# Kernel tuning notes

Measured on AMD Instinct MI355X. Metric: run time of the kernel, lower is better.

The kernel has to match this reference:

```python
import jax, jax.numpy as jnp
import numpy as np

STRIDES = (8.0, 16.0, 32.0)


def _decode_level(feat, W, b, stride, level):
    # feat: [bs, C, ny, nx]; W: [85, C]; b: [85]
    bs, _, ny, nx = feat.shape
    # 1x1 conv == channel contraction; output laid out as [bs, ny, nx, 85]
    p = jnp.einsum('bchw,oc->bhwo', feat, W) + b
    y = jax.nn.sigmoid(p)
    xv = jnp.arange(nx, dtype=y.dtype)            # broadcasts over last spatial dim
    yv = jnp.arange(ny, dtype=y.dtype)[:, None]   # broadcasts over row dim
    power = jnp.asarray(2.0 ** level, dtype=y.dtype)
    d = (y[..., :4] * 2.0) ** 2 * power           # dx1, dy1, dx2, dy2
    x1 = (xv + 1.0 - d[..., 0]) * stride
    y1 = (yv + 1.0 - d[..., 1]) * stride
    x2 = (xv + d[..., 2]) * stride
    y2 = (yv + d[..., 3]) * stride
    # xyxy -> xywh
    box = jnp.stack([(x1 + x2) * 0.5, (y1 + y2) * 0.5, x2 - x1, y2 - y1], axis=-1)
    out = jnp.concatenate([box, y[..., 4:]], axis=-1)  # [bs, ny, nx, 85]
    return out.reshape(bs, ny * nx, out.shape[-1])


def setup_inputs() -> dict:
    key = jax.random.key(0)
    ks = jax.random.split(key, 9)
    f32 = jnp.float32
    return {
        'x0': jax.random.normal(ks[0], (16, 256, 80, 80), dtype=f32),
        'x1': jax.random.normal(ks[1], (16, 512, 40, 40), dtype=f32),
        'x2': jax.random.normal(ks[2], (16, 1024, 20, 20), dtype=f32),
        'W0': jax.random.normal(ks[3], (85, 256), dtype=f32) * 0.05,
        'b0': jax.random.normal(ks[4], (85,), dtype=f32) * 0.05,
        'W1': jax.random.normal(ks[5], (85, 512), dtype=f32) * 0.05,
        'b1': jax.random.normal(ks[6], (85,), dtype=f32) * 0.05,
        'W2': jax.random.normal(ks[7], (85, 1024), dtype=f32) * 0.05,
        'b2': jax.random.normal(ks[8], (85,), dtype=f32) * 0.05,
    }


def reference(x0, x1, x2, W0, b0, W1, b1, W2, b2):
    feats = (x0, x1, x2)
    Ws = (W0, W1, W2)
    bs_ = (b0, b1, b2)
    z = [_decode_level(feats[i], Ws[i], bs_[i], STRIDES[i], i) for i in range(3)]
    return jnp.concatenate(z, axis=1)  # [bs, 8400, 85]
```

## Files before the change

kernel.cpp:

```cpp
#include <hip/hip_runtime.h>
#include <cstdint>


typedef __attribute__((ext_vector_type(8))) short bf16x8;
typedef __attribute__((ext_vector_type(4))) float f32x4;

constexpr int KS0 = 8, KS1 = 16, KS2 = 32;
constexpr int F0 = 6 * KS0, F1 = 6 * KS1, F2 = 6 * KS2;
constexpr int FOFF0 = 0, FOFF1 = F0, FOFF2 = F0 + F1;
constexpr int NFRAG = F0 + F1 + F2;
constexpr size_t BIAS_OFF = 0;
constexpr size_t BPK_OFF  = 1152;
constexpr size_t WS_NEED  = BPK_OFF + (size_t)NFRAG * 64 * 16;

__device__ __forceinline__ unsigned short f2bf(float f) {
    union { float f; unsigned u; } v; v.f = f;
    unsigned r = v.u + 0x7FFF + ((v.u >> 16) & 1);
    return (unsigned short)(r >> 16);
}

__global__ __launch_bounds__(256) void prep_pack(
    const float* __restrict__ W0, const float* __restrict__ W1,
    const float* __restrict__ W2,
    const float* __restrict__ b0, const float* __restrict__ b1,
    const float* __restrict__ b2,
    unsigned char* __restrict__ ws)
{
    int t = blockIdx.x * 256 + threadIdx.x;
    if (t < 288) {
        int lvl = t / 96, o = t % 96;
        const float* bp = (lvl == 0) ? b0 : (lvl == 1) ? b1 : b2;
        ((float*)(ws + BIAS_OFF))[t] = (o < 85) ? bp[o] : 0.0f;
    }
    if (t >= NFRAG * 64) return;
    int frag = t >> 6, l = t & 63;
    int C; const float* W; int f;
    if (frag < FOFF1)      { C = 256;  W = W0; f = frag;         }
    else if (frag < FOFF2) { C = 512;  W = W1; f = frag - FOFF1; }
    else                   { C = 1024; W = W2; f = frag - FOFF2; }
    int ks = f / 6, n = f % 6;
    int o  = n * 16 + (l & 15);
    int c0 = ks * 32 + (l >> 4) * 8;
    bf16x8 r;
#pragma unroll
    for (int e = 0; e < 8; ++e)
        r[e] = (o < 85) ? (short)f2bf(W[(size_t)o * C + c0 + e]) : (short)0;
    ((bf16x8*)(ws + BPK_OFF))[frag * 64 + l] = r;
}

template <int C, int HW, int NX, int LEVEL, int AOFF, int KSTEPS, int FOFF>
__device__ __forceinline__ void mfma_level(
    const float* __restrict__ feat, const unsigned char* __restrict__ ws,
    float* __restrict__ out, int blk, uint4* __restrict__ Bsm )
{
    const int tid = threadIdx.x;
    const int w   = tid >> 6;
    const int l   = tid & 63;
    const int col = l & 15;
    const int kg  = l >> 4;

    const int p0s[2] = { blk * 128 + w * 32, blk * 128 + w * 32 + 16 };
    const float* fb[2];
    int bidx[2], hw0[2];
#pragma unroll
    for (int s = 0; s < 2; ++s) {
        int b   = p0s[s] / HW;
        bidx[s] = b;
        hw0[s]  = p0s[s] - b * HW;
        fb[s]   = feat + (size_t)b * C * HW + hw0[s];
    }

    const float* bias = (const float*)(ws + BIAS_OFF) + LEVEL * 96;
    const uint4* bsrc = (const uint4*)(ws + BPK_OFF) + (size_t)FOFF * 64;

    f32x4 acc[2][6];
#pragma unroll
    for (int n = 0; n < 6; ++n) {
        float bv = bias[n * 16 + col];
        f32x4 z = { bv, bv, bv, bv };
        acc[0][n] = z;
        acc[1][n] = z;
    }

    {
        const uint4* s = bsrc;
        Bsm[tid] = s[tid];
        if (tid < 128) Bsm[256 + tid] = s[256 + tid];
    }
    __syncthreads();

    int cur = 0;
    for (int ks = 0; ks < KSTEPS; ++ks) {
        float fl0[8], fl1[8];
        const float* p0p = fb[0] + col + (size_t)(ks * 32 + kg * 8) * HW;
        const float* p1p = fb[1] + col + (size_t)(ks * 32 + kg * 8) * HW;
#pragma unroll
        for (int e = 0; e < 8; ++e) fl0[e] = p0p[(size_t)e * HW];
#pragma unroll
        for (int e = 0; e < 8; ++e) fl1[e] = p1p[(size_t)e * HW];

        uint4 s0, s1;
        const int ksn = (ks + 1 < KSTEPS) ? ks + 1 : ks;
        {
            const uint4* s = bsrc + (size_t)ksn * 384;
            s0 = s[tid];
            if (tid < 128) s1 = s[256 + tid];
        }

        bf16x8 a0, a1;
#pragma unroll
        for (int e = 0; e < 8; ++e) a0[e] = (short)f2bf(fl0[e]);
#pragma unroll
        for (int e = 0; e < 8; ++e) a1[e] = (short)f2bf(fl1[e]);

        const bf16x8* bl = (const bf16x8*)(Bsm + (size_t)cur * 384);
#pragma unroll
        for (int n = 0; n < 6; ++n) {
            bf16x8 bq = bl[n * 64 + l];
            acc[0][n] = __builtin_amdgcn_mfma_f32_16x16x32_bf16(a0, bq, acc[0][n], 0, 0, 0);
            acc[1][n] = __builtin_amdgcn_mfma_f32_16x16x32_bf16(a1, bq, acc[1][n], 0, 0, 0);
        }

        if (ks + 1 < KSTEPS) {
            uint4* d = Bsm + (size_t)(cur ^ 1) * 384;
            d[tid] = s0;
            if (tid < 128) d[256 + tid] = s1;
        }
        __syncthreads();
        cur ^= 1;
    }

    constexpr float S  = (float)(8 << LEVEL);
    constexpr float P4 = 4.0f * (float)(1 << LEVEL);
#pragma unroll
    for (int s = 0; s < 2; ++s) {
        const int b = bidx[s];
#pragma unroll
        for (int j = 0; j < 4; ++j) {
            const int hw = hw0[s] + kg * 4 + j;
            float sg[6];
#pragma unroll
            for (int n = 0; n < 6; ++n) {
                float v = acc[s][n][j];
                sg[n] = __builtin_amdgcn_rcpf(1.0f + __expf(-v));
            }
            const int grp = l & 48;
            float y0 = __shfl(sg[0], grp + 0);
            float y1 = __shfl(sg[0], grp + 1);
            float y2 = __shfl(sg[0], grp + 2);
            float y3 = __shfl(sg[0], grp + 3);
            float wx = (float)(hw % NX);
            float wy = (float)(hw / NX);
            float d0 = y0 * y0 * P4, d1 = y1 * y1 * P4;
            float d2 = y2 * y2 * P4, d3 = y3 * y3 * P4;
            float x1 = (wx + 1.0f - d0) * S;
            float yA = (wy + 1.0f - d1) * S;
            float x2 = (wx + d2) * S;
            float yB = (wy + d3) * S;
            float bx = (x1 + x2) * 0.5f, by = (yA + yB) * 0.5f;
            float bw = x2 - x1,          bh = yB - yA;
            sg[0] = (col == 0) ? bx : (col == 1) ? by
                  : (col == 2) ? bw : (col == 3) ? bh : sg[0];
            float* op = out + ((size_t)b * 8400 + AOFF + hw) * 85;
#pragma unroll
            for (int n = 0; n < 6; ++n) {
                int o = n * 16 + col;
                if (o < 85) op[o] = sg[n];
            }
        }
    }
}

__global__ __launch_bounds__(256, 4) void detect_mfma(
    const float* __restrict__ x0, const float* __restrict__ x1,
    const float* __restrict__ x2,
    const unsigned char* __restrict__ ws, float* __restrict__ out)
{
    __shared__ uint4 Bsm[2 * 384];
    int blk = blockIdx.x;
    if (blk < 50)       mfma_level<1024, 400,  20, 2, 8000, KS2, FOFF2>(x2, ws, out, blk,       Bsm);
    else if (blk < 250) mfma_level<512,  1600, 40, 1, 6400, KS1, FOFF1>(x1, ws, out, blk - 50,  Bsm);
    else                mfma_level<256,  6400, 80, 0, 0,    KS0, FOFF0>(x0, ws, out, blk - 250, Bsm);
}

template <int C, int HW, int NX, int LEVEL, int ONUM, bool BOX>
__device__ __forceinline__ void decode_path_fb(
    const float* __restrict__ feat, const float* __restrict__ Wm,
    const float* __restrict__ bias, float* __restrict__ out,
    int o_lo_in, int pos)
{
    const int o_lo = __builtin_amdgcn_readfirstlane(o_lo_in);
    const int b  = pos / HW;
    const int hw = pos - b * HW;
    const float* fp = feat + (size_t)b * (C * HW) + hw;
    float acc[ONUM];
#pragma unroll
    for (int j = 0; j < ONUM; ++j) acc[j] = bias[o_lo + j];
#pragma unroll 4
    for (int c = 0; c < C; ++c) {
        float fv = fp[(size_t)c * HW];
#pragma unroll
        for (int j = 0; j < ONUM; ++j)
            acc[j] = fmaf(fv, Wm[(o_lo + j) * C + c], acc[j]);
    }
#pragma unroll
    for (int j = 0; j < ONUM; ++j)
        acc[j] = __builtin_amdgcn_rcpf(1.0f + __expf(-acc[j]));
    constexpr float S = (float)(8 << LEVEL);
    constexpr int AOFF = (LEVEL == 0) ? 0 : ((LEVEL == 1) ? 6400 : 8000);
    float* op = out + ((size_t)b * 8400 + AOFF + hw) * 85 + o_lo;
    if constexpr (BOX) {
        constexpr float P4 = 4.0f * (float)(1 << LEVEL);
        float wx = (float)(hw % NX), wy = (float)(hw / NX);
        float d0 = acc[0] * acc[0] * P4, d1 = acc[1] * acc[1] * P4;
        float d2 = acc[2] * acc[2] * P4, d3 = acc[3] * acc[3] * P4;
        float x1 = (wx + 1.0f - d0) * S, y1 = (wy + 1.0f - d1) * S;
        float x2 = (wx + d2) * S,        y2 = (wy + d3) * S;
        op[0] = (x1 + x2) * 0.5f; op[1] = (y1 + y2) * 0.5f;
        op[2] = x2 - x1;          op[3] = y2 - y1;
#pragma unroll
        for (int j = 4; j < ONUM; ++j) op[j] = acc[j];
    } else {
#pragma unroll
        for (int j = 0; j < ONUM; ++j) op[j] = acc[j];
    }
}

template <int C, int HW, int NX, int LEVEL>
__device__ __forceinline__ void level_block_fb(
    const float* __restrict__ feat, const float* __restrict__ Wm,
    const float* __restrict__ bias, float* __restrict__ out, int bb)
{
    const int wave = threadIdx.x >> 6, lane = threadIdx.x & 63;
    const int pos = bb * 64 + lane;
    if      (wave == 0) decode_path_fb<C, HW, NX, LEVEL, 22, true >(feat, Wm, bias, out, 0,  pos);
    else if (wave == 1) decode_path_fb<C, HW, NX, LEVEL, 22, false>(feat, Wm, bias, out, 22, pos);
    else if (wave == 2) decode_path_fb<C, HW, NX, LEVEL, 22, false>(feat, Wm, bias, out, 44, pos);
    else                decode_path_fb<C, HW, NX, LEVEL, 19, false>(feat, Wm, bias, out, 66, pos);
}

__global__ __launch_bounds__(256) void detect_fallback(
    const float* __restrict__ x0, const float* __restrict__ x1,
    const float* __restrict__ x2,
    const float* __restrict__ w0, const float* __restrict__ w1,
    const float* __restrict__ w2,
    const float* __restrict__ b0, const float* __restrict__ b1,
    const float* __restrict__ b2, float* __restrict__ out)
{
    const int blk = blockIdx.x;
    if (blk < 100)      level_block_fb<1024, 400,  20, 2>(x2, w2, b2, out, blk);
    else if (blk < 500) level_block_fb<512,  1600, 40, 1>(x1, w1, b1, out, blk - 100);
    else                level_block_fb<256,  6400, 80, 0>(x0, w0, b0, out, blk - 500);
}

extern "C" void kernel_launch(void* const* d_in, const int* in_sizes, int n_in,
                              void* d_out, int out_size, void* d_ws, size_t ws_size,
                              hipStream_t stream)
{
    const float* x0 = (const float*)d_in[0];
    const float* x1 = (const float*)d_in[1];
    const float* x2 = (const float*)d_in[2];
    const float* W0 = (const float*)d_in[3];
    const float* b0 = (const float*)d_in[4];
    const float* W1 = (const float*)d_in[5];
    const float* b1 = (const float*)d_in[6];
    const float* W2 = (const float*)d_in[7];
    const float* b2 = (const float*)d_in[8];
    float* out = (float*)d_out;

    if (ws_size >= WS_NEED) {
        unsigned char* ws = (unsigned char*)d_ws;
        prep_pack<<<(NFRAG * 64 + 255) / 256, 256, 0, stream>>>(W0, W1, W2, b0, b1, b2, ws);
        detect_mfma<<<1050, 256, 0, stream>>>(x0, x1, x2, ws, out);
    } else {
        detect_fallback<<<2100, 256, 0, stream>>>(x0, x1, x2, W0, W1, W2, b0, b1, b2, out);
    }
}
```

Before: 52.57 us.

## Halve positions per wave, prefetch next activations, double grid and occupancy

Each wave now handles one 16-position tile instead of two, so the grid doubles to 2100 blocks and launch bounds ask for 6 blocks per CU instead of 4. Activation loads for the next K-step are software-prefetched into registers while the current step's MFMAs run. The aim is more parallelism and better latency hiding on this memory-bound contraction. The cost is that each packed weight fragment staged into LDS is now reused by half as many MFMAs, which doubles weight traffic per output.

```diff
diff --git a/kernel.cpp b/kernel.cpp
--- a/kernel.cpp
+++ b/kernel.cpp
@@ -59,27 +59,20 @@
     const int col = l & 15;
     const int kg  = l >> 4;
 
-    const int p0s[2] = { blk * 128 + w * 32, blk * 128 + w * 32 + 16 };
-    const float* fb[2];
-    int bidx[2], hw0[2];
-#pragma unroll
-    for (int s = 0; s < 2; ++s) {
-        int b   = p0s[s] / HW;
-        bidx[s] = b;
-        hw0[s]  = p0s[s] - b * HW;
-        fb[s]   = feat + (size_t)b * C * HW + hw0[s];
-    }
+    const int p0  = blk * 64 + w * 16;
+    const int b   = p0 / HW;
+    const int hw0 = p0 - b * HW;
+    const float* fb = feat + (size_t)b * C * HW + hw0;
 
     const float* bias = (const float*)(ws + BIAS_OFF) + LEVEL * 96;
     const uint4* bsrc = (const uint4*)(ws + BPK_OFF) + (size_t)FOFF * 64;
 
-    f32x4 acc[2][6];
+    f32x4 acc[6];
 #pragma unroll
     for (int n = 0; n < 6; ++n) {
         float bv = bias[n * 16 + col];
         f32x4 z = { bv, bv, bv, bv };
-        acc[0][n] = z;
-        acc[1][n] = z;
+        acc[n] = z;
     }
 
     {
@@ -87,44 +80,47 @@
         Bsm[tid] = s[tid];
         if (tid < 128) Bsm[256 + tid] = s[256 + tid];
     }
+    float fl_cur[8];
+    {
+        const float* p = fb + col + (size_t)(kg * 8) * HW;
+#pragma unroll
+        for (int e = 0; e < 8; ++e) fl_cur[e] = p[(size_t)e * HW];
+    }
     __syncthreads();
 
     int cur = 0;
     for (int ks = 0; ks < KSTEPS; ++ks) {
-        float fl0[8], fl1[8];
-        const float* p0p = fb[0] + col + (size_t)(ks * 32 + kg * 8) * HW;
-        const float* p1p = fb[1] + col + (size_t)(ks * 32 + kg * 8) * HW;
-#pragma unroll
-        for (int e = 0; e < 8; ++e) fl0[e] = p0p[(size_t)e * HW];
-#pragma unroll
-        for (int e = 0; e < 8; ++e) fl1[e] = p1p[(size_t)e * HW];
+        float fl_next[8];
+        if (ks + 1 < KSTEPS) {
+            const float* p = fb + col + (size_t)((ks + 1) * 32 + kg * 8) * HW;
+#pragma unroll
+            for (int e = 0; e < 8; ++e) fl_next[e] = p[(size_t)e * HW];
+        }
 
         uint4 s0, s1;
-        const int ksn = (ks + 1 < KSTEPS) ? ks + 1 : ks;
-        {
-            const uint4* s = bsrc + (size_t)ksn * 384;
+        if (ks + 1 < KSTEPS) {
+            const uint4* s = bsrc + (size_t)(ks + 1) * 384;
             s0 = s[tid];
             if (tid < 128) s1 = s[256 + tid];
         }
 
-        bf16x8 a0, a1;
-#pragma unroll
-        for (int e = 0; e < 8; ++e) a0[e] = (short)f2bf(fl0[e]);
-#pragma unroll
-        for (int e = 0; e < 8; ++e) a1[e] = (short)f2bf(fl1[e]);
+        bf16x8 a;
+#pragma unroll
+        for (int e = 0; e < 8; ++e) a[e] = (short)f2bf(fl_cur[e]);
 
         const bf16x8* bl = (const bf16x8*)(Bsm + (size_t)cur * 384);
 #pragma unroll
         for (int n = 0; n < 6; ++n) {
             bf16x8 bq = bl[n * 64 + l];
-            acc[0][n] = __builtin_amdgcn_mfma_f32_16x16x32_bf16(a0, bq, acc[0][n], 0, 0, 0);
-            acc[1][n] = __builtin_amdgcn_mfma_f32_16x16x32_bf16(a1, bq, acc[1][n], 0, 0, 0);
+            acc[n] = __builtin_amdgcn_mfma_f32_16x16x32_bf16(a, bq, acc[n], 0, 0, 0);
         }
 
         if (ks + 1 < KSTEPS) {
             uint4* d = Bsm + (size_t)(cur ^ 1) * 384;
             d[tid] = s0;
             if (tid < 128) d[256 + tid] = s1;
+#pragma unroll
+            for (int e = 0; e < 8; ++e) fl_cur[e] = fl_next[e];
         }
         __syncthreads();
         cur ^= 1;
@@ -133,54 +129,50 @@
     constexpr float S  = (float)(8 << LEVEL);
     constexpr float P4 = 4.0f * (float)(1 << LEVEL);
 #pragma unroll
-    for (int s = 0; s < 2; ++s) {
-        const int b = bidx[s];
-#pragma unroll
-        for (int j = 0; j < 4; ++j) {
-            const int hw = hw0[s] + kg * 4 + j;
-            float sg[6];
-#pragma unroll
-            for (int n = 0; n < 6; ++n) {
-                float v = acc[s][n][j];
-                sg[n] = __builtin_amdgcn_rcpf(1.0f + __expf(-v));
-            }
-            const int grp = l & 48;
-            float y0 = __shfl(sg[0], grp + 0);
-            float y1 = __shfl(sg[0], grp + 1);
-            float y2 = __shfl(sg[0], grp + 2);
-            float y3 = __shfl(sg[0], grp + 3);
-            float wx = (float)(hw % NX);
-            float wy = (float)(hw / NX);
-            float d0 = y0 * y0 * P4, d1 = y1 * y1 * P4;
-            float d2 = y2 * y2 * P4, d3 = y3 * y3 * P4;
-            float x1 = (wx + 1.0f - d0) * S;
-            float yA = (wy + 1.0f - d1) * S;
-            float x2 = (wx + d2) * S;
-            float yB = (wy + d3) * S;
-            float bx = (x1 + x2) * 0.5f, by = (yA + yB) * 0.5f;
-            float bw = x2 - x1,          bh = yB - yA;
-            sg[0] = (col == 0) ? bx : (col == 1) ? by
-                  : (col == 2) ? bw : (col == 3) ? bh : sg[0];
-            float* op = out + ((size_t)b * 8400 + AOFF + hw) * 85;
-#pragma unroll
-            for (int n = 0; n < 6; ++n) {
-                int o = n * 16 + col;
-                if (o < 85) op[o] = sg[n];
-            }
-        }
-    }
-}
-
-__global__ __launch_bounds__(256, 4) void detect_mfma(
+    for (int j = 0; j < 4; ++j) {
+        const int hw = hw0 + kg * 4 + j;
+        float sg[6];
+#pragma unroll
+        for (int n = 0; n < 6; ++n) {
+            float v = acc[n][j];
+            sg[n] = __builtin_amdgcn_rcpf(1.0f + __expf(-v));
+        }
+        const int grp = l & 48;
+        float y0 = __shfl(sg[0], grp + 0);
+        float y1 = __shfl(sg[0], grp + 1);
+        float y2 = __shfl(sg[0], grp + 2);
+        float y3 = __shfl(sg[0], grp + 3);
+        float wx = (float)(hw % NX);
+        float wy = (float)(hw / NX);
+        float d0 = y0 * y0 * P4, d1 = y1 * y1 * P4;
+        float d2 = y2 * y2 * P4, d3 = y3 * y3 * P4;
+        float x1 = (wx + 1.0f - d0) * S;
+        float yA = (wy + 1.0f - d1) * S;
+        float x2 = (wx + d2) * S;
+        float yB = (wy + d3) * S;
+        float bx = (x1 + x2) * 0.5f, by = (yA + yB) * 0.5f;
+        float bw = x2 - x1,          bh = yB - yA;
+        sg[0] = (col == 0) ? bx : (col == 1) ? by
+              : (col == 2) ? bw : (col == 3) ? bh : sg[0];
+        float* op = out + ((size_t)b * 8400 + AOFF + hw) * 85;
+#pragma unroll
+        for (int n = 0; n < 6; ++n) {
+            int o = n * 16 + col;
+            if (o < 85) op[o] = sg[n];
+        }
+    }
+}
+
+__global__ __launch_bounds__(256, 6) void detect_mfma(
     const float* __restrict__ x0, const float* __restrict__ x1,
     const float* __restrict__ x2,
     const unsigned char* __restrict__ ws, float* __restrict__ out)
 {
     __shared__ uint4 Bsm[2 * 384];
     int blk = blockIdx.x;
-    if (blk < 50)       mfma_level<1024, 400,  20, 2, 8000, KS2, FOFF2>(x2, ws, out, blk,       Bsm);
-    else if (blk < 250) mfma_level<512,  1600, 40, 1, 6400, KS1, FOFF1>(x1, ws, out, blk - 50,  Bsm);
-    else                mfma_level<256,  6400, 80, 0, 0,    KS0, FOFF0>(x0, ws, out, blk - 250, Bsm);
+    if (blk < 100)      mfma_level<1024, 400,  20, 2, 8000, KS2, FOFF2>(x2, ws, out, blk,       Bsm);
+    else if (blk < 500) mfma_level<512,  1600, 40, 1, 6400, KS1, FOFF1>(x1, ws, out, blk - 100, Bsm);
+    else                mfma_level<256,  6400, 80, 0, 0,    KS0, FOFF0>(x0, ws, out, blk - 500, Bsm);
 }
 
 template <int C, int HW, int NX, int LEVEL, int ONUM, bool BOX>
@@ -271,7 +263,7 @@
     if (ws_size >= WS_NEED) {
         unsigned char* ws = (unsigned char*)d_ws;
         prep_pack<<<(NFRAG * 64 + 255) / 256, 256, 0, stream>>>(W0, W1, W2, b0, b1, b2, ws);
-        detect_mfma<<<1050, 256, 0, stream>>>(x0, x1, x2, ws, out);
+        detect_mfma<<<2100, 256, 0, stream>>>(x0, x1, x2, ws, out);
     } else {
         detect_fallback<<<2100, 256, 0, stream>>>(x0, x1, x2, W0, W1, W2, b0, b1, b2, out);
     }
```

New measurement: 47.90 us. -8.9%, faster.
